# Performance work log

Measured on AMD Instinct MI355X. Metric: run time of the kernel, lower is better.

Reference implementation:

```python
import jax, jax.numpy as jnp
import numpy as np

N_STREAKS = 40  # fixed draw from num_streaks=(20, 60)


def setup_inputs() -> dict:
    key = jax.random.key(0)
    k1, k2, k3, k4, k5 = jax.random.split(key, 5)
    B, C, H, W = 32, 3, 512, 512
    x = jax.random.uniform(k1, (B, C, H, W), dtype=jnp.float32)  # images in [0,1]
    # alpha ~ U(0.15, 0.5) as in the module
    alpha = 0.15 + 0.35 * jax.random.uniform(k2, (1,), dtype=jnp.float32)
    xc = jax.random.randint(k3, (N_STREAKS,), 0, W)            # column center in [0, W-1]
    y0 = jax.random.randint(k4, (N_STREAKS,), 0, H // 2 + 1)   # top in [0, H/2]
    y1_off = jax.random.randint(k5, (N_STREAKS,), 0, H // 2 + 1)  # y1 = H/2 + y1_off in [H/2, H]
    return {"x": x, "alpha": alpha, "xc": xc, "y0": y0, "y1_off": y1_off}


def reference(x, alpha, xc, y0, y1_off):
    # Each streak applies v -> v*(1-a) + a on its rectangle; repeated k times this is
    # v*(1-a)^k + (1 - (1-a)^k), which is order-independent, so we rasterize an
    # overlap-count map K[H,W] and apply the closed-form blend in one fused pass.
    B, C, H, W = x.shape
    a = alpha[0]
    y1 = y1_off + H // 2
    rows = jnp.arange(H)
    cols = jnp.arange(W)
    row_mask = (rows[None, :] >= y0[:, None]) & (rows[None, :] < y1[:, None])  # [n, H]
    c0 = jnp.maximum(xc - 1, 0)
    col_mask = (cols[None, :] >= c0[:, None]) & (cols[None, :] < (xc + 1)[:, None])  # [n, W]
    K = jnp.einsum('nh,nw->hw', row_mask.astype(x.dtype), col_mask.astype(x.dtype))  # [H, W]
    f = jnp.power(1.0 - a, K)  # (1-a)^K, broadcast over B, C
    out = jnp.clip(x * f + (1.0 - f), 0.0, 1.0)
    return out
```

## Files before the change

kernel.cpp:

```cpp
#include <hip/hip_runtime.h>

#define IMG_H 512
#define IMG_W 512
#define MAX_STREAKS 64
#define ROWS_PER_BLOCK 8

typedef float v4f __attribute__((ext_vector_type(4)));

__device__ __forceinline__ v4f blend4(v4f xv, v4f fv) {
    v4f o;
    o.x = fminf(fmaxf(fmaf(xv.x, fv.x, 1.0f - fv.x), 0.0f), 1.0f);
    o.y = fminf(fmaxf(fmaf(xv.y, fv.y, 1.0f - fv.y), 0.0f), 1.0f);
    o.z = fminf(fmaxf(fmaf(xv.z, fv.z, 1.0f - fv.z), 0.0f), 1.0f);
    o.w = fminf(fmaxf(fmaf(xv.w, fv.w, 1.0f - fv.w), 0.0f), 1.0f);
    return o;
}

__global__ void __launch_bounds__(256)
rain_fused_kernel(const v4f* __restrict__ x,
                  const float* __restrict__ alpha,
                  const int* __restrict__ xc,
                  const int* __restrict__ y0,
                  const int* __restrict__ y1_off,
                  v4f* __restrict__ out,
                  int n_streaks) {
    __shared__ int s_xc[MAX_STREAKS], s_y0[MAX_STREAKS], s_y1[MAX_STREAKS];
    __shared__ float s_f[ROWS_PER_BLOCK][IMG_W];
    int* s_hist = (int*)&s_f[0][0];

    const int tid = threadIdx.x;
    if (tid < n_streaks) {
        s_xc[tid] = xc[tid];
        s_y0[tid] = y0[tid];
        s_y1[tid] = y1_off[tid] + IMG_H / 2;
    }
    #pragma unroll
    for (int i = tid; i < ROWS_PER_BLOCK * IMG_W; i += 256) s_hist[i] = 0;
    __syncthreads();

    const int hbase = (blockIdx.x * ROWS_PER_BLOCK) & (IMG_H - 1);

    for (int p = tid; p < (n_streaks << 3); p += 256) {
        int r = p & 7, s = p >> 3;
        int h = hbase + r;
        if (h >= s_y0[s] && h < s_y1[s]) {
            int c = s_xc[s];
            atomicAdd(&s_hist[(r << 9) + (c - 1 > 0 ? c - 1 : 0)], 1);
            if (c >= 1) atomicAdd(&s_hist[(r << 9) + c], 1);
        }
    }
    __syncthreads();

    const float l2f = __log2f(1.0f - alpha[0]);
    #pragma unroll
    for (int i = tid; i < ROWS_PER_BLOCK * IMG_W; i += 256) {
        int k = s_hist[i];
        ((float*)s_hist)[i] = exp2f(l2f * (float)k);
    }
    __syncthreads();

    const v4f* xb = x + (size_t)blockIdx.x * 1024;
    v4f*       ob = out + (size_t)blockIdx.x * 1024;
    const v4f* fb = (const v4f*)&s_f[0][0];
    #pragma unroll
    for (int k = 0; k < 4; ++k) {
        int idx = (k << 8) + tid;
        v4f xv = xb[idx];
        v4f fv = fb[idx];
        __builtin_nontemporal_store(blend4(xv, fv), &ob[idx]);
    }
}

extern "C" void kernel_launch(void* const* d_in, const int* in_sizes, int n_in,
                              void* d_out, int out_size, void* d_ws, size_t ws_size,
                              hipStream_t stream) {
    const float* x      = (const float*)d_in[0];
    const float* alpha  = (const float*)d_in[1];
    const int*   xc     = (const int*)d_in[2];
    const int*   y0     = (const int*)d_in[3];
    const int*   y1_off = (const int*)d_in[4];
    float* out = (float*)d_out;

    int n_streaks = in_sizes[2];

    int blocks = out_size / (ROWS_PER_BLOCK * IMG_W);
    rain_fused_kernel<<<blocks, 256, 0, stream>>>(
        (const v4f*)x, alpha, xc, y0, y1_off, (v4f*)out, n_streaks);
}
```

Measured before the change: 36.36 us.

## Reuse per-row blend factors across four image slices per block

Each block now computes the 8-row factor map once and applies it to four (batch,channel) slices, where before it was rebuilt for every slice. The grid shrinks by four and the histogram, exp2 and shared-memory setup work is amortized. The factor values are held in registers and the clear and exp2 loops are vectorized to float4. This gives fewer blocks and fewer resident waves with which to hide memory latency.

```diff
diff --git a/kernel.cpp b/kernel.cpp
--- a/kernel.cpp
+++ b/kernel.cpp
@@ -4,8 +4,10 @@
 #define IMG_W 512
 #define MAX_STREAKS 64
 #define ROWS_PER_BLOCK 8
+#define SLICES_PER_BLOCK 4
 
 typedef float v4f __attribute__((ext_vector_type(4)));
+typedef int   v4i __attribute__((ext_vector_type(4)));
 
 __device__ __forceinline__ v4f blend4(v4f xv, v4f fv) {
     v4f o;
@@ -26,6 +28,7 @@
                   int n_streaks) {
     __shared__ int s_xc[MAX_STREAKS], s_y0[MAX_STREAKS], s_y1[MAX_STREAKS];
     __shared__ float s_f[ROWS_PER_BLOCK][IMG_W];
+    v4f* s_f4 = (v4f*)&s_f[0][0];
     int* s_hist = (int*)&s_f[0][0];
 
     const int tid = threadIdx.x;
@@ -35,10 +38,15 @@
         s_y1[tid] = y1_off[tid] + IMG_H / 2;
     }
     #pragma unroll
-    for (int i = tid; i < ROWS_PER_BLOCK * IMG_W; i += 256) s_hist[i] = 0;
+    for (int i = tid; i < ROWS_PER_BLOCK * IMG_W / 4; i += 256) {
+        v4f z = {0.0f, 0.0f, 0.0f, 0.0f};
+        s_f4[i] = z;
+    }
     __syncthreads();
 
-    const int hbase = (blockIdx.x * ROWS_PER_BLOCK) & (IMG_H - 1);
+    const int rc = blockIdx.x & 63;
+    const int grp = blockIdx.x >> 6;
+    const int hbase = rc * ROWS_PER_BLOCK;
 
     for (int p = tid; p < (n_streaks << 3); p += 256) {
         int r = p & 7, s = p >> 3;
@@ -53,21 +61,36 @@
 
     const float l2f = __log2f(1.0f - alpha[0]);
     #pragma unroll
-    for (int i = tid; i < ROWS_PER_BLOCK * IMG_W; i += 256) {
-        int k = s_hist[i];
-        ((float*)s_hist)[i] = exp2f(l2f * (float)k);
+    for (int i = tid; i < ROWS_PER_BLOCK * IMG_W / 4; i += 256) {
+        v4i kv = *(v4i*)&s_f4[i];
+        v4f fv;
+        fv.x = exp2f(l2f * (float)kv.x);
+        fv.y = exp2f(l2f * (float)kv.y);
+        fv.z = exp2f(l2f * (float)kv.z);
+        fv.w = exp2f(l2f * (float)kv.w);
+        s_f4[i] = fv;
     }
     __syncthreads();
 
-    const v4f* xb = x + (size_t)blockIdx.x * 1024;
-    v4f*       ob = out + (size_t)blockIdx.x * 1024;
-    const v4f* fb = (const v4f*)&s_f[0][0];
+    v4f f0 = s_f4[tid];
+    v4f f1 = s_f4[256 + tid];
+    v4f f2 = s_f4[512 + tid];
+    v4f f3 = s_f4[768 + tid];
+
+    const size_t base = (size_t)grp * SLICES_PER_BLOCK * (IMG_H * IMG_W / 4)
+                      + (size_t)rc * (ROWS_PER_BLOCK * IMG_W / 4);
     #pragma unroll
-    for (int k = 0; k < 4; ++k) {
-        int idx = (k << 8) + tid;
-        v4f xv = xb[idx];
-        v4f fv = fb[idx];
-        __builtin_nontemporal_store(blend4(xv, fv), &ob[idx]);
+    for (int j = 0; j < SLICES_PER_BLOCK; ++j) {
+        const v4f* xb = x   + base + (size_t)j * (IMG_H * IMG_W / 4);
+        v4f*       ob = out + base + (size_t)j * (IMG_H * IMG_W / 4);
+        v4f x0 = xb[tid];
+        v4f x1 = xb[256 + tid];
+        v4f x2 = xb[512 + tid];
+        v4f x3 = xb[768 + tid];
+        __builtin_nontemporal_store(blend4(x0, f0), &ob[tid]);
+        __builtin_nontemporal_store(blend4(x1, f1), &ob[256 + tid]);
+        __builtin_nontemporal_store(blend4(x2, f2), &ob[512 + tid]);
+        __builtin_nontemporal_store(blend4(x3, f3), &ob[768 + tid]);
     }
 }
 
@@ -83,7 +106,7 @@
 
     int n_streaks = in_sizes[2];
 
-    int blocks = out_size / (ROWS_PER_BLOCK * IMG_W);
+    int blocks = out_size / (ROWS_PER_BLOCK * IMG_W * SLICES_PER_BLOCK);
     rain_fused_kernel<<<blocks, 256, 0, stream>>>(
         (const v4f*)x, alpha, xc, y0, y1_off, (v4f*)out, n_streaks);
 }
```

After: 36.84 us. Within noise of the previous version (+1.3%).
